# Kernel optimization log

Measured on AMD Instinct MI355X. Metric: run time of the kernel, lower is better.

## Reference

```python
import jax, jax.numpy as jnp
import numpy as np

NUM_CAPSULE = 32
DIM_VECTOR = 16
NUM_ROUTING = 3

def squash(v, axis=-1):
    s2 = jnp.sum(jnp.square(v), axis=axis, keepdims=True)
    scale = s2 / (1.0 + s2) / jnp.sqrt(s2)
    return scale * v

def setup_inputs() -> dict:
    key = jax.random.key(0)
    k1, k2 = jax.random.split(key)
    B, IN_CAPS, IN_DIM = 64, 2048, 8
    x = jax.random.normal(k1, (B, IN_CAPS, IN_DIM), dtype=jnp.float32)
    # glorot-uniform-ish weight: [in_caps, num_caps, in_dim, out_dim]
    limit = np.sqrt(6.0 / (IN_DIM + DIM_VECTOR)).astype(np.float32)
    W = jax.random.uniform(k2, (IN_CAPS, NUM_CAPSULE, IN_DIM, DIM_VECTOR), dtype=jnp.float32, minval=-limit, maxval=limit)
    return {"x": x, "W": W}

def reference(x, W):
    # x: [B, in_caps, in_dim]; W: [in_caps, num_caps, in_dim, out_dim]
    # inputs_hat (u_hat): [B, in_caps, num_caps, out_dim]
    u_hat = jnp.einsum('bid,inde->bine', x, W)
    B, IN_CAPS = u_hat.shape[0], u_hat.shape[1]
    # routing logits; original broadcasts over out_dim with identical values,
    # so a trailing singleton dim is mathematically equivalent
    b = jnp.zeros((B, IN_CAPS, NUM_CAPSULE, 1), dtype=u_hat.dtype)
    v = None
    for i in range(NUM_ROUTING):
        c = jax.nn.softmax(b, axis=2)                       # over num_capsule
        s = jnp.sum(c * u_hat, axis=1, keepdims=True)       # [B,1,nc,out]
        v = squash(s)                                       # [B,1,nc,out]
        if i != NUM_ROUTING - 1:
            b = b + jnp.sum(u_hat * v, axis=-1, keepdims=True)
    return v.reshape(-1, NUM_CAPSULE, DIM_VECTOR)
```

## Files before the change

### kernel.cpp

```cpp
#include <hip/hip_runtime.h>
#include <math.h>


#define B_TOT 64
#define I_TOT 2048
#define D_IN  8
#define NC    32
#define EV    16
#define OD    (NC*EV)
#define BC    8
#define NBC   (B_TOT/BC)
#define ICH   8
#define NIC   (I_TOT/ICH)

__device__ __forceinline__ void fma4(float4& acc, float a, const float4& w) {
    acc.x = fmaf(a, w.x, acc.x);
    acc.y = fmaf(a, w.y, acc.y);
    acc.z = fmaf(a, w.z, acc.z);
    acc.w = fmaf(a, w.w, acc.w);
}

template <int MODE>
__global__ __launch_bounds__(256, 4)
void route_pass(const float* __restrict__ x, const float* __restrict__ W,
                float* __restrict__ P, const float* __restrict__ vin)
{
    __shared__ __align__(16) float xl[BC * ICH * D_IN];
    __shared__ float wsum[2][4][BC];

    const int t  = threadIdx.x;
    const int ic = blockIdx.x & (NIC - 1);
    const int bc = blockIdx.x >> 8;
    const int b0 = bc * BC;
    const int i0 = ic * ICH;
    const int eq = t & 3;
    const int bh = (t >> 2) & 1;
    const int n  = t >> 3;
    const int w  = t >> 6;

    if (t < 128) {
        const int row = t >> 4, f = (t & 15) * 4;
        *(float4*)&xl[row * (ICH * D_IN) + f] =
            *(const float4*)&x[((size_t)(b0 + row) * I_TOT + i0) * D_IN + f];
    }

    float4 vr[4];
    if (MODE == 1) {
        #pragma unroll
        for (int q = 0; q < 4; ++q)
            vr[q] = *(const float4*)&vin[(size_t)(b0 + bh * 4 + q) * OD + n * EV + eq * 4];
    }
    __syncthreads();

    float4 sacc[4];
    #pragma unroll
    for (int q = 0; q < 4; ++q) sacc[q] = make_float4(0.f, 0.f, 0.f, 0.f);

    const float* Wt = &W[(size_t)i0 * 4096 + n * 128 + eq * 4];

    #pragma unroll 1
    for (int ii = 0; ii < ICH; ++ii) {
        float4 wr[8];
        #pragma unroll
        for (int d = 0; d < 8; ++d)
            wr[d] = *(const float4*)&Wt[ii * 4096 + d * 16];

        float4 u[4];
        #pragma unroll
        for (int q = 0; q < 4; ++q) {
            const int bl = bh * 4 + q;
            float4 xa = *(float4*)&xl[bl * (ICH * D_IN) + ii * 8];
            float4 xb = *(float4*)&xl[bl * (ICH * D_IN) + ii * 8 + 4];
            float4 uu = make_float4(0.f, 0.f, 0.f, 0.f);
            fma4(uu, xa.x, wr[0]); fma4(uu, xa.y, wr[1]);
            fma4(uu, xa.z, wr[2]); fma4(uu, xa.w, wr[3]);
            fma4(uu, xb.x, wr[4]); fma4(uu, xb.y, wr[5]);
            fma4(uu, xb.z, wr[6]); fma4(uu, xb.w, wr[7]);
            u[q] = uu;
        }

        if (MODE == 0) {
            #pragma unroll
            for (int q = 0; q < 4; ++q) {
                sacc[q].x += u[q].x; sacc[q].y += u[q].y;
                sacc[q].z += u[q].z; sacc[q].w += u[q].w;
            }
        } else {
            float a[4];
            #pragma unroll
            for (int q = 0; q < 4; ++q) {
                float ap = u[q].x * vr[q].x + u[q].y * vr[q].y
                         + u[q].z * vr[q].z + u[q].w * vr[q].w;
                ap += __shfl_xor(ap, 1, 64);
                ap += __shfl_xor(ap, 2, 64);
                a[q] = ap;
            }
            float e[4], p[4];
            #pragma unroll
            for (int q = 0; q < 4; ++q) {
                e[q] = __expf(a[q]);
                float pp = e[q];
                pp += __shfl_xor(pp, 8, 64);
                pp += __shfl_xor(pp, 16, 64);
                pp += __shfl_xor(pp, 32, 64);
                p[q] = pp;
            }
            if (eq == 0) {
                #pragma unroll
                for (int q = 0; q < 4; ++q)
                    wsum[ii & 1][w][bh * 4 + q] = p[q];
            }
            __syncthreads();
            #pragma unroll
            for (int q = 0; q < 4; ++q) {
                const int bl = bh * 4 + q;
                float s = wsum[ii & 1][0][bl] + wsum[ii & 1][1][bl]
                        + wsum[ii & 1][2][bl] + wsum[ii & 1][3][bl];
                float c = e[q] / s;
                fma4(sacc[q], c, u[q]);
            }
        }
    }

    #pragma unroll
    for (int q = 0; q < 4; ++q)
        *(float4*)&P[((size_t)ic * B_TOT + b0 + bh * 4 + q) * OD + n * EV + eq * 4] = sacc[q];
}

__global__ __launch_bounds__(256, 4)
void reduce_squash(const float* __restrict__ P, float* __restrict__ dst,
                   const float* __restrict__ addsrc, float pre)
{
    __shared__ float red[256];
    const int b   = blockIdx.x >> 3;
    const int oq  = blockIdx.x & 7;
    const int t   = threadIdx.x;
    const int o   = oq * 64 + (t & 63);
    const int icq = t >> 6;
    const size_t stride = (size_t)B_TOT * OD;

    float s = 0.f;
    size_t base = ((size_t)(icq * 64) * B_TOT + b) * OD + o;
    #pragma unroll 8
    for (int k = 0; k < 64; ++k) s += P[base + (size_t)k * stride];
    red[t] = s;
    __syncthreads();

    if (t < 64) {
        float v = red[t] + red[t + 64] + red[t + 128] + red[t + 192];
        v *= pre;
        float q2 = v * v;
        q2 += __shfl_xor(q2, 1, 64);
        q2 += __shfl_xor(q2, 2, 64);
        q2 += __shfl_xor(q2, 4, 64);
        q2 += __shfl_xor(q2, 8, 64);
        float sc = q2 / ((1.0f + q2) * sqrtf(q2));
        float outv = v * sc;
        if (addsrc) outv += addsrc[b * OD + o];
        dst[b * OD + o] = outv;
    }
}

extern "C" void kernel_launch(void* const* d_in, const int* in_sizes, int n_in,
                              void* d_out, int out_size, void* d_ws, size_t ws_size,
                              hipStream_t stream) {
    const float* x = (const float*)d_in[0];
    const float* W = (const float*)d_in[1];
    float* out = (float*)d_out;

    char* ws = (char*)d_ws;
    float* P  = (float*)ws;
    float* v0 = (float*)(ws + (size_t)32 * 1024 * 1024);
    float* vs = v0 + B_TOT * OD;

    dim3 rg(NBC * NIC), rb(256);
    dim3 sg(B_TOT * 8), sb(256);

    route_pass<0><<<rg, rb, 0, stream>>>(x, W, P, nullptr);
    reduce_squash<<<sg, sb, 0, stream>>>(P, v0, nullptr, 1.0f / 32.0f);
    route_pass<1><<<rg, rb, 0, stream>>>(x, W, P, v0);
    reduce_squash<<<sg, sb, 0, stream>>>(P, vs, v0, 1.0f);
    route_pass<1><<<rg, rb, 0, stream>>>(x, W, P, vs);
    reduce_squash<<<sg, sb, 0, stream>>>(P, out, nullptr, 1.0f);
}
```

Measured before the change: 196.4 us.

## Double-buffer W tiles in LDS via async global_load_lds prefetch

The routing kernel now streams each input capsule's W slice into a swizzled, double-buffered LDS region using async global-to-LDS loads. The next capsule's slice is prefetched while the current one is computed, with explicit vmcnt waits in place of direct global-to-register loads. Each wave fetches only the W rows it later reads, so no cross-wave barrier is needed for the buffer. The softmax barrier is also replaced with an explicit lgkmcnt wait plus s_barrier. This adds 32KB of LDS per block, which may limit occupancy, and relies on hand-counted vmcnt values that assume no other outstanding vector-memory loads are in flight.

```diff
diff --git a/kernel.cpp b/kernel.cpp
--- a/kernel.cpp
+++ b/kernel.cpp
@@ -20,11 +20,19 @@
     acc.w = fmaf(a, w.w, acc.w);
 }
 
+__device__ __forceinline__ void gload_lds16(const float* g, float* l) {
+    __builtin_amdgcn_global_load_lds(
+        (const __attribute__((address_space(1))) unsigned int*)g,
+        (__attribute__((address_space(3))) unsigned int*)l,
+        16, 0, 0);
+}
+
 template <int MODE>
 __global__ __launch_bounds__(256, 4)
 void route_pass(const float* __restrict__ x, const float* __restrict__ W,
                 float* __restrict__ P, const float* __restrict__ vin)
 {
+    __shared__ __align__(16) float wbuf[2][4096];
     __shared__ __align__(16) float xl[BC * ICH * D_IN];
     __shared__ float wsum[2][4][BC];
 
@@ -37,6 +45,23 @@
     const int bh = (t >> 2) & 1;
     const int n  = t >> 3;
     const int w  = t >> 6;
+    const int lane = t & 63;
+
+    int soff[4];
+    #pragma unroll
+    for (int j = 0; j < 4; ++j) {
+        const int ns   = w * 8 + j * 2 + (lane >> 5);
+        const int slot = (lane >> 2) & 7;
+        const int eqs  = lane & 3;
+        const int d    = slot ^ (ns & 7);
+        soff[j] = ns * 128 + d * 16 + eqs * 4;
+    }
+    const float* Wic = W + (size_t)i0 * 4096;
+    const int wdst = w * 1024;
+
+    #pragma unroll
+    for (int j = 0; j < 4; ++j)
+        gload_lds16(Wic + soff[j], &wbuf[0][wdst + j * 256]);
 
     if (t < 128) {
         const int row = t >> 4, f = (t & 15) * 4;
@@ -56,14 +81,26 @@
     #pragma unroll
     for (int q = 0; q < 4; ++q) sacc[q] = make_float4(0.f, 0.f, 0.f, 0.f);
 
-    const float* Wt = &W[(size_t)i0 * 4096 + n * 128 + eq * 4];
+    const int nx = n & 7;
+    const int rbase = n * 128 + eq * 4;
 
     #pragma unroll 1
     for (int ii = 0; ii < ICH; ++ii) {
+        const int cur = ii & 1;
+        if (ii + 1 < ICH) {
+            const float* ws = Wic + (size_t)(ii + 1) * 4096;
+            #pragma unroll
+            for (int j = 0; j < 4; ++j)
+                gload_lds16(ws + soff[j], &wbuf[cur ^ 1][wdst + j * 256]);
+            asm volatile("s_waitcnt vmcnt(4)" ::: "memory");
+        } else {
+            asm volatile("s_waitcnt vmcnt(0)" ::: "memory");
+        }
+
         float4 wr[8];
         #pragma unroll
         for (int d = 0; d < 8; ++d)
-            wr[d] = *(const float4*)&Wt[ii * 4096 + d * 16];
+            wr[d] = *(const float4*)&wbuf[cur][rbase + ((d ^ nx) << 4)];
 
         float4 u[4];
         #pragma unroll
@@ -108,14 +145,14 @@
             if (eq == 0) {
                 #pragma unroll
                 for (int q = 0; q < 4; ++q)
-                    wsum[ii & 1][w][bh * 4 + q] = p[q];
-            }
-            __syncthreads();
+                    wsum[cur][w][bh * 4 + q] = p[q];
+            }
+            asm volatile("s_waitcnt lgkmcnt(0)\n\ts_barrier" ::: "memory");
             #pragma unroll
             for (int q = 0; q < 4; ++q) {
                 const int bl = bh * 4 + q;
-                float s = wsum[ii & 1][0][bl] + wsum[ii & 1][1][bl]
-                        + wsum[ii & 1][2][bl] + wsum[ii & 1][3][bl];
+                float s = wsum[cur][0][bl] + wsum[cur][1][bl]
+                        + wsum[cur][2][bl] + wsum[cur][3][bl];
                 float c = e[q] / s;
                 fma4(sacc[q], c, u[q]);
             }
```

Result: slower. 200.5 us (+2.1%).
